# Kernel tuning notes

Measured on AMD Instinct MI355X. Metric: run time of the kernel, lower is better.

Reference implementation:

```python
import jax, jax.numpy as jnp
import numpy as np

B, C, T, V, P = 32, 64, 512, 54, 4
EPS = 1e-5


def setup_inputs() -> dict:
    key = jax.random.key(0)
    ks = jax.random.split(key, 5)
    x = jax.random.normal(ks[0], (B, C, T, V), dtype=jnp.float32)
    A = jax.random.uniform(ks[1], (P, V, V), dtype=jnp.float32)
    gweights = jax.random.normal(ks[2], (P, V, V), dtype=jnp.float32)
    W = jax.random.normal(ks[3], (P, C, C), dtype=jnp.float32) * 0.05  # (P, C_out, C_in)
    b = jax.random.normal(ks[4], (P, C), dtype=jnp.float32) * 0.05
    gamma = jnp.ones((C,), dtype=jnp.float32)
    beta = jnp.zeros((C,), dtype=jnp.float32)
    return {"x": x, "A": A, "gweights": gweights, "W": W, "b": b,
            "gamma": gamma, "beta": beta}


def reference(x, A, gweights, W, b, gamma, beta):
    # x: (B, C_in, T, V)
    Aeff = A * gweights  # (P, V, V), learned-weighted adjacency
    # per-part graph aggregation (x @ A_p) followed by 1x1 conv, summed over parts
    # out[b,o,t,v] = sum_p sum_c sum_u x[b,c,t,u] * Aeff[p,u,v] * W[p,o,c] + sum_p b[p,o]
    y = jnp.einsum('bctu,puv,poc->botv', x, Aeff, W, optimize=True)
    y = y + jnp.sum(b, axis=0)[None, :, None, None]
    # BatchNorm2d in training mode: batch stats over (B, T, V) per channel
    mean = jnp.mean(y, axis=(0, 2, 3), keepdims=True)
    var = jnp.mean(jnp.square(y - mean), axis=(0, 2, 3), keepdims=True)
    y = (y - mean) * jax.lax.rsqrt(var + EPS)
    y = y * gamma[None, :, None, None] + beta[None, :, None, None]
    y = jax.nn.relu(y)
    # temporal_conv is Identity (kernel_size=None); residual shortcut is Identity (C_in==C_out)
    return y + x
```

## Files before the change

### kernel.cpp

```cpp
#include <hip/hip_runtime.h>
#include <hip/hip_bf16.h>


typedef __bf16 bf16_t;
typedef __bf16 bf16x8 __attribute__((ext_vector_type(8)));
typedef __bf16 bf16x4 __attribute__((ext_vector_type(4)));
typedef float  f32x4  __attribute__((ext_vector_type(4)));
typedef unsigned int uint32;

static __device__ __forceinline__ f32x4 mfma16(bf16x8 a, bf16x8 b, f32x4 c) {
  return __builtin_amdgcn_mfma_f32_16x16x32_bf16(a, b, c, 0, 0, 0);
}
static __device__ __forceinline__ uint32 pk2(float a, float b) {
  union { __bf16 h; unsigned short u; } ua, ub;
  ua.h = (__bf16)a; ub.h = (__bf16)b;
  return (uint32)ua.u | ((uint32)ub.u << 16);
}
static __device__ __forceinline__ float bflo(uint32 u) {
  union { uint32 u; float f; } r; r.u = u << 16; return r.f;
}
static __device__ __forceinline__ float bfhi(uint32 u) {
  union { uint32 u; float f; } r; r.u = u & 0xffff0000u; return r.f;
}

__global__ __launch_bounds__(256) void k_prep(
    const float* __restrict__ A, const float* __restrict__ g,
    const float* __restrict__ W, const float* __restrict__ bias,
    bf16_t* __restrict__ W2, bf16_t* __restrict__ Ae,
    float* __restrict__ bsum, float* __restrict__ stats) {
  int i = blockIdx.x * 256 + threadIdx.x;
  if (i < 16384) {
    int o = i >> 8, k = i & 255, p = k >> 6, c = k & 63;
    W2[i] = (bf16_t)W[p * 4096 + o * 64 + c];
  }
  if (i < 224 * 64) {
    int pv = i >> 6, u = i & 63;
    int p = pv / 56, v = pv - p * 56;
    float val = 0.f;
    if (v < 54 && u < 54) {
      int idx = (p * 54 + u) * 54 + v;
      val = A[idx] * g[idx];
    }
    Ae[i] = (bf16_t)val;
  }
  if (i < 64) {
    float s = 0.f;
    for (int p = 0; p < 4; ++p) s += bias[p * 64 + i];
    bsum[i] = s;
  }
  if (i < 8192) stats[i] = 0.f;
}

__global__ __launch_bounds__(256) void k_cast(const float* __restrict__ x,
                                              bf16_t* __restrict__ xbf) {
  const size_t i = (size_t)blockIdx.x * 256 + threadIdx.x;
  const float4 a = ((const float4*)x)[2 * i];
  const float4 b = ((const float4*)x)[2 * i + 1];
  union { uint32 u[4]; uint4 v; } r;
  r.u[0] = pk2(a.x, a.y); r.u[1] = pk2(a.z, a.w);
  r.u[2] = pk2(b.x, b.y); r.u[3] = pk2(b.z, b.w);
  ((uint4*)xbf)[i] = r.v;
}

#define ZS  264
#define XSS 72

__global__ __launch_bounds__(256, 3) void k_pass1_bf(
    const bf16_t* __restrict__ xbf, const bf16_t* __restrict__ W2,
    const bf16_t* __restrict__ Ae, const float* __restrict__ bsum,
    bf16_t* __restrict__ yprev, float* __restrict__ stats) {
  __shared__ bf16_t Zt[64 * ZS];
  __shared__ bf16_t Xs[64 * XSS];
  __shared__ __align__(16) bf16_t Ys[64 * 54];

  const int tid  = threadIdx.x;
  const int bid  = blockIdx.x;
  const int b    = bid >> 7;
  const int t0   = (bid & 127) << 2;
  const int w    = tid >> 6;
  const int L    = tid & 63;
  const int quad = L >> 4;
  const int l15  = L & 15;

  for (int i = tid; i < 8 * ZS / 2; i += 256)
    ((uint32*)(Zt + 56 * ZS))[i] = 0u;

  bf16x8 wf[8];
  #pragma unroll
  for (int kk = 0; kk < 8; ++kk)
    wf[kk] = *(const bf16x8*)(W2 + (((w << 4) + l15) << 8) + (kk << 5) + (quad << 3));

  int zoff[14];
  #pragma unroll
  for (int n = 0; n < 14; ++n) {
    int pv = (n << 4) + l15;
    int p = pv / 56;
    int v = pv - p * 56;
    zoff[n] = v * ZS + (p << 6) + (w << 4) + (quad << 2);
  }

  const int oc  = (w << 4) + l15;
  const float bsv = bsum[oc];
  float ssum = 0.f, ssq = 0.f;

  const int  f2   = tid & 31;
  const bool ldon = f2 < 27;
  const bf16_t* xgb = xbf + ((size_t)(b << 6) + (tid >> 5)) * 27648 + (f2 << 1);
  uint32* xsd = (uint32*)((char*)Xs + (tid >> 5) * (XSS * 2) + (f2 << 2));

  uint32 pfu[8];
  #pragma unroll
  for (int j = 0; j < 8; ++j) pfu[j] = 0u;
  if (ldon) {
    #pragma unroll
    for (int j = 0; j < 8; ++j)
      pfu[j] = *(const uint32*)(xgb + (size_t)j * 221184 + (size_t)t0 * 54);
  }

  for (int tt = 0; tt < 4; ++tt) {
    const int t = t0 + tt;

    #pragma unroll
    for (int j = 0; j < 8; ++j) xsd[j * 288] = pfu[j];

    __syncthreads();

    const bf16_t* xr = Xs + oc * XSS;
    bf16x8 xa0 = *(const bf16x8*)(xr + (quad << 3));
    bf16x8 xa1 = *(const bf16x8*)(xr + 32 + (quad << 3));
    #pragma unroll
    for (int n = 0; n < 14; ++n) {
      const bf16_t* ar = Ae + (((n << 4) + l15) << 6) + (quad << 3);
      f32x4 acc = {0.f, 0.f, 0.f, 0.f};
      acc = mfma16(xa0, *(const bf16x8*)(ar), acc);
      acc = mfma16(xa1, *(const bf16x8*)(ar + 32), acc);
      uint32* dst = (uint32*)(Zt + zoff[n]);
      dst[0] = pk2(acc[0], acc[1]);
      dst[1] = pk2(acc[2], acc[3]);
    }

    __syncthreads();

    if (ldon && tt < 3) {
      #pragma unroll
      for (int j = 0; j < 8; ++j)
        pfu[j] = *(const uint32*)(xgb + (size_t)j * 221184 + (size_t)(t + 1) * 54);
    }

    #pragma unroll
    for (int mi = 0; mi < 4; ++mi) {
      f32x4 acc = {0.f, 0.f, 0.f, 0.f};
      #pragma unroll
      for (int kk = 0; kk < 8; ++kk) {
        bf16x8 za = *(const bf16x8*)(Zt + ((mi << 4) + l15) * ZS
                                        + (kk << 5) + (quad << 3));
        acc = mfma16(za, wf[kk], acc);
      }
      const int v0 = (mi << 4) + (quad << 2);
      if (v0 + 3 < 54) {
        float y0 = acc[0] + bsv, y1 = acc[1] + bsv, y2 = acc[2] + bsv, y3 = acc[3] + bsv;
        uint32* d = (uint32*)(Ys + oc * 54 + v0);
        d[0] = pk2(y0, y1); d[1] = pk2(y2, y3);
        ssum += y0 + y1 + y2 + y3;
        ssq  += y0 * y0 + y1 * y1 + y2 * y2 + y3 * y3;
      } else if (v0 == 52) {
        float y0 = acc[0] + bsv, y1 = acc[1] + bsv;
        *(uint32*)(Ys + oc * 54 + v0) = pk2(y0, y1);
        ssum += y0 + y1;
        ssq  += y0 * y0 + y1 * y1;
      }
    }

    __syncthreads();
    const uint4* ys4 = (const uint4*)Ys;
    uint4* yp4 = (uint4*)((uint32*)yprev + (size_t)bid * 6912 + (size_t)tt * 1728);
    yp4[tid] = ys4[tid];
    if (tid < 176) yp4[256 + tid] = ys4[256 + tid];
  }

  ssum += __shfl_xor(ssum, 16); ssq += __shfl_xor(ssq, 16);
  ssum += __shfl_xor(ssum, 32); ssq += __shfl_xor(ssq, 32);
  if (L < 16) {
    float* sb = stats + (bid & 63) * 128;
    atomicAdd(&sb[oc], ssum);
    atomicAdd(&sb[64 + oc], ssq);
  }
}

__global__ __launch_bounds__(256, 3) void k_pass1_fp32(
    const float* __restrict__ x, const bf16_t* __restrict__ W2,
    const bf16_t* __restrict__ Ae, const float* __restrict__ bsum,
    float* __restrict__ yprev, float* __restrict__ stats) {
  __shared__ bf16_t Zt[64 * ZS];
  __shared__ bf16_t Xs[64 * XSS];

  const int tid  = threadIdx.x;
  const int bid  = blockIdx.x;
  const int b    = bid >> 7;
  const int t0   = (bid & 127) << 2;
  const int w    = tid >> 6;
  const int L    = tid & 63;
  const int quad = L >> 4;
  const int l15  = L & 15;

  for (int i = tid; i < 8 * ZS / 2; i += 256)
    ((uint32*)(Zt + 56 * ZS))[i] = 0u;

  bf16x8 wf[8];
  #pragma unroll
  for (int kk = 0; kk < 8; ++kk)
    wf[kk] = *(const bf16x8*)(W2 + (((w << 4) + l15) << 8) + (kk << 5) + (quad << 3));

  int zoff[14];
  #pragma unroll
  for (int n = 0; n < 14; ++n) {
    int pv = (n << 4) + l15;
    int p = pv / 56;
    int v = pv - p * 56;
    zoff[n] = v * ZS + (p << 6) + (w << 4) + (quad << 2);
  }

  const int oc  = (w << 4) + l15;
  const float bsv = bsum[oc];
  float ssum = 0.f, ssq = 0.f;

  const int  f2   = tid & 31;
  const bool ldon = f2 < 27;
  const size_t gbase = ((size_t)(b << 6) + (tid >> 5)) * 27648 + ((size_t)f2 << 1);
  uint32* xsd = (uint32*)((char*)Xs + (tid >> 5) * (XSS * 2) + (f2 << 2));

  float2 pf[8];
  #pragma unroll
  for (int j = 0; j < 8; ++j) pf[j] = make_float2(0.f, 0.f);
  if (ldon) {
    #pragma unroll
    for (int j = 0; j < 8; ++j)
      pf[j] = *(const float2*)(x + gbase + (size_t)j * 221184 + (size_t)t0 * 54);
  }

  for (int tt = 0; tt < 4; ++tt) {
    const int t = t0 + tt;
    #pragma unroll
    for (int j = 0; j < 8; ++j) xsd[j * 288] = pk2(pf[j].x, pf[j].y);
    __syncthreads();

    const bf16_t* xr = Xs + oc * XSS;
    bf16x8 xa0 = *(const bf16x8*)(xr + (quad << 3));
    bf16x8 xa1 = *(const bf16x8*)(xr + 32 + (quad << 3));
    #pragma unroll
    for (int n = 0; n < 14; ++n) {
      const bf16_t* ar = Ae + (((n << 4) + l15) << 6) + (quad << 3);
      f32x4 acc = {0.f, 0.f, 0.f, 0.f};
      acc = mfma16(xa0, *(const bf16x8*)(ar), acc);
      acc = mfma16(xa1, *(const bf16x8*)(ar + 32), acc);
      uint32* dst = (uint32*)(Zt + zoff[n]);
      dst[0] = pk2(acc[0], acc[1]);
      dst[1] = pk2(acc[2], acc[3]);
    }
    __syncthreads();

    if (ldon && tt < 3) {
      #pragma unroll
      for (int j = 0; j < 8; ++j)
        pf[j] = *(const float2*)(x + gbase + (size_t)j * 221184 + (size_t)(t + 1) * 54);
    }

    const size_t obase = (((size_t)((b << 6) + oc) << 9) + (size_t)t) * 54;
    #pragma unroll
    for (int mi = 0; mi < 4; ++mi) {
      f32x4 acc = {0.f, 0.f, 0.f, 0.f};
      #pragma unroll
      for (int kk = 0; kk < 8; ++kk) {
        bf16x8 za = *(const bf16x8*)(Zt + ((mi << 4) + l15) * ZS
                                        + (kk << 5) + (quad << 3));
        acc = mfma16(za, wf[kk], acc);
      }
      const int v0 = (mi << 4) + (quad << 2);
      if (v0 + 3 < 54) {
        float y0 = acc[0] + bsv, y1 = acc[1] + bsv, y2 = acc[2] + bsv, y3 = acc[3] + bsv;
        float2* d = (float2*)(yprev + obase + v0);
        d[0] = make_float2(y0, y1); d[1] = make_float2(y2, y3);
        ssum += y0 + y1 + y2 + y3;
        ssq  += y0 * y0 + y1 * y1 + y2 * y2 + y3 * y3;
      } else if (v0 == 52) {
        float y0 = acc[0] + bsv, y1 = acc[1] + bsv;
        *(float2*)(yprev + obase + v0) = make_float2(y0, y1);
        ssum += y0 + y1;
        ssq  += y0 * y0 + y1 * y1;
      }
    }
    __syncthreads();
  }

  ssum += __shfl_xor(ssum, 16); ssq += __shfl_xor(ssq, 16);
  ssum += __shfl_xor(ssum, 32); ssq += __shfl_xor(ssq, 32);
  if (L < 16) {
    float* sb = stats + (bid & 63) * 128;
    atomicAdd(&sb[oc], ssum);
    atomicAdd(&sb[64 + oc], ssq);
  }
}

__global__ void k_finalize(const float* __restrict__ gamma, const float* __restrict__ beta,
                           const float* __restrict__ stats, float* __restrict__ ac) {
  int o = threadIdx.x;
  if (o >= 64) return;
  float S = 0.f, Q = 0.f;
  for (int buf = 0; buf < 64; ++buf) {
    S += stats[buf * 128 + o];
    Q += stats[buf * 128 + 64 + o];
  }
  const float inv = 1.0f / 884736.0f;
  float mean = S * inv;
  float var  = Q * inv - mean * mean;
  float a = gamma[o] * rsqrtf(var + 1e-5f);
  ac[o] = a;
  ac[64 + o] = beta[o] - mean * a;
}

__global__ __launch_bounds__(256) void k_pass2_lin(
    const float* __restrict__ x, const float* __restrict__ ac,
    const void* __restrict__ yprev, float* __restrict__ out) {
  __shared__ float acS[128];
  const int tid = threadIdx.x;
  const int bid = blockIdx.x;
  if (tid < 128) acS[tid] = ac[tid];
  __syncthreads();

  const int b  = bid >> 7;
  const int t0 = (bid & 127) << 2;
  const uint32* yp = (const uint32*)yprev + (size_t)bid * 6912;
  const float* xb  = x + (size_t)b * 1769472;
  float* ob        = out + (size_t)b * 1769472;

  #pragma unroll 3
  for (int k = 0; k < 27; ++k) {
    const int d  = (k << 8) + tid;
    const int e0 = d << 1;
    const unsigned tt = (unsigned)e0 / 3456u;
    const unsigned r  = (unsigned)e0 - tt * 3456u;
    const unsigned ocv = r / 54u;
    const unsigned v   = r - ocv * 54u;
    const uint32 u = yp[d];
    const float a = acS[ocv], cc = acS[64 + ocv];
    const size_t xi = (size_t)ocv * 27648 + (size_t)(t0 + tt) * 54 + v;
    const float2 xv = *(const float2*)(xb + xi);
    float2 o2;
    o2.x = fmaxf(fmaf(a, bflo(u), cc), 0.f) + xv.x;
    o2.y = fmaxf(fmaf(a, bfhi(u), cc), 0.f) + xv.y;
    *(float2*)(ob + xi) = o2;
  }
}

__global__ __launch_bounds__(256) void k_pass2_fb(const float* __restrict__ x,
                                                  const float* __restrict__ ac,
                                                  const float* __restrict__ yprev,
                                                  float* __restrict__ out) {
  const int slab = blockIdx.y;
  const int o = slab & 63;
  const size_t base = (size_t)slab * 27648 + (size_t)(((blockIdx.x << 8) + threadIdx.x) << 2);
  const float a = ac[o], c = ac[64 + o];
  float4 yp = *(const float4*)(yprev + base);
  float4 xv = *(const float4*)(x + base);
  float4 r;
  r.x = fmaxf(fmaf(a, yp.x, c), 0.f) + xv.x;
  r.y = fmaxf(fmaf(a, yp.y, c), 0.f) + xv.y;
  r.z = fmaxf(fmaf(a, yp.z, c), 0.f) + xv.z;
  r.w = fmaxf(fmaf(a, yp.w, c), 0.f) + xv.w;
  *(float4*)(out + base) = r;
}

extern "C" void kernel_launch(void* const* d_in, const int* in_sizes, int n_in,
                              void* d_out, int out_size, void* d_ws, size_t ws_size,
                              hipStream_t stream) {
  const float* x     = (const float*)d_in[0];
  const float* A     = (const float*)d_in[1];
  const float* g     = (const float*)d_in[2];
  const float* W     = (const float*)d_in[3];
  const float* bias  = (const float*)d_in[4];
  const float* gamma = (const float*)d_in[5];
  const float* beta  = (const float*)d_in[6];

  char* ws = (char*)d_ws;
  bf16_t* W2    = (bf16_t*)(ws + 0);
  bf16_t* Ae    = (bf16_t*)(ws + 32768);
  float*  bsum  = (float*)(ws + 61440);
  float*  stats = (float*)(ws + 61696);
  float*  ac    = (float*)(ws + 94464);
  const size_t XBF_OFF   = 98304;
  const size_t XBF_BYTES = (size_t)32 * 64 * 512 * 54 * 2;
  const size_t YP_OFF    = XBF_OFF + XBF_BYTES;
  float* out = (float*)d_out;

  k_prep<<<64, 256, 0, stream>>>(A, g, W, bias, W2, Ae, bsum, stats);

  if (ws_size >= YP_OFF + XBF_BYTES + 4096) {
    bf16_t* xbf  = (bf16_t*)(ws + XBF_OFF);
    bf16_t* ypre = (bf16_t*)(ws + YP_OFF);
    k_cast<<<27648, 256, 0, stream>>>(x, xbf);
    k_pass1_bf<<<4096, 256, 0, stream>>>(xbf, W2, Ae, bsum, ypre, stats);
    k_finalize<<<1, 64, 0, stream>>>(gamma, beta, stats, ac);
    k_pass2_lin<<<4096, 256, 0, stream>>>(x, ac, ypre, out);
  } else {
    k_pass1_fp32<<<4096, 256, 0, stream>>>(x, W2, Ae, bsum, out, stats);
    k_finalize<<<1, 64, 0, stream>>>(gamma, beta, stats, ac);
    k_pass2_fb<<<dim3(27, 2048), 256, 0, stream>>>(x, ac, out, out);
  }
}
```

Baseline: 717.8 us.

## Cast x into per-block contiguous tiles and shrink pass1 to two timesteps

The cast kernel now writes x in bf16 into contiguous per-block tiles of 64 channels by 2 timesteps, so pass1 can load its whole input slab with coalesced 16-byte loads instead of strided per-channel gathers and register prefetch. Pass1 now handles 2 timesteps per block across 8192 blocks and writes y directly to global memory, dropping the LDS staging buffer and its copy-out. This cuts shared memory and sync overhead but gives up the prefetch overlap. The cast now does strided float2 reads, and the direct y stores are narrower and less coalesced.

Result: slower. 792.5 us (+10.4%).

```diff
diff --git a/kernel.cpp b/kernel.cpp
--- a/kernel.cpp
+++ b/kernel.cpp
@@ -51,38 +51,58 @@
   if (i < 8192) stats[i] = 0.f;
 }
 
-__global__ __launch_bounds__(256) void k_cast(const float* __restrict__ x,
-                                              bf16_t* __restrict__ xbf) {
-  const size_t i = (size_t)blockIdx.x * 256 + threadIdx.x;
-  const float4 a = ((const float4*)x)[2 * i];
-  const float4 b = ((const float4*)x)[2 * i + 1];
-  union { uint32 u[4]; uint4 v; } r;
-  r.u[0] = pk2(a.x, a.y); r.u[1] = pk2(a.z, a.w);
-  r.u[2] = pk2(b.x, b.y); r.u[3] = pk2(b.z, b.w);
-  ((uint4*)xbf)[i] = r.v;
-}
-
-#define ZS  264
-#define XSS 72
-
-__global__ __launch_bounds__(256, 3) void k_pass1_bf(
-    const bf16_t* __restrict__ xbf, const bf16_t* __restrict__ W2,
+__global__ __launch_bounds__(256) void k_cast_blk(const float* __restrict__ x,
+                                                  bf16_t* __restrict__ xblk) {
+  const int tid = threadIdx.x;
+  const int bid = blockIdx.x;
+  const int b   = bid >> 8;
+  const int t0  = (bid & 255) << 1;
+  const float* xb = x + (size_t)b * 1769472;
+  uint32* dstD = (uint32*)xblk + (size_t)bid * 3456;
+  #pragma unroll
+  for (int r = 0; r < 7; ++r) {
+    int d = (r << 8) + tid;
+    if (d < 1728) {
+      int c  = d / 27;
+      int u2 = d - c * 27;
+      const float* s = xb + (size_t)c * 27648 + (size_t)t0 * 54 + (u2 << 1);
+      float2 a0 = *(const float2*)s;
+      float2 a1 = *(const float2*)(s + 54);
+      dstD[d]        = pk2(a0.x, a0.y);
+      dstD[d + 1728] = pk2(a1.x, a1.y);
+    }
+  }
+}
+
+#define ZS 264
+
+__global__ __launch_bounds__(256, 3) void k_pass1_blk(
+    const bf16_t* __restrict__ xblk, const bf16_t* __restrict__ W2,
     const bf16_t* __restrict__ Ae, const float* __restrict__ bsum,
     bf16_t* __restrict__ yprev, float* __restrict__ stats) {
+  __shared__ __align__(16) bf16_t Xs[2 * 64 * 54 + 64];
   __shared__ bf16_t Zt[64 * ZS];
-  __shared__ bf16_t Xs[64 * XSS];
-  __shared__ __align__(16) bf16_t Ys[64 * 54];
 
   const int tid  = threadIdx.x;
   const int bid  = blockIdx.x;
-  const int b    = bid >> 7;
-  const int t0   = (bid & 127) << 2;
+  const int b    = bid >> 8;
+  const int t0   = (bid & 255) << 1;
   const int w    = tid >> 6;
   const int L    = tid & 63;
   const int quad = L >> 4;
   const int l15  = L & 15;
 
-  for (int i = tid; i < 8 * ZS / 2; i += 256)
+  {
+    const uint4* src = (const uint4*)(xblk + (size_t)bid * 6912);
+    uint4* xs4 = (uint4*)Xs;
+    #pragma unroll
+    for (int r = 0; r < 4; ++r) {
+      int i4 = (r << 8) + tid;
+      if (i4 < 864) xs4[i4] = src[i4];
+    }
+  }
+
+  for (int i = tid; i < 1056; i += 256)
     ((uint32*)(Zt + 56 * ZS))[i] = 0u;
 
   bf16x8 wf[8];
@@ -103,31 +123,21 @@
   const float bsv = bsum[oc];
   float ssum = 0.f, ssq = 0.f;
 
-  const int  f2   = tid & 31;
-  const bool ldon = f2 < 27;
-  const bf16_t* xgb = xbf + ((size_t)(b << 6) + (tid >> 5)) * 27648 + (f2 << 1);
-  uint32* xsd = (uint32*)((char*)Xs + (tid >> 5) * (XSS * 2) + (f2 << 2));
-
-  uint32 pfu[8];
-  #pragma unroll
-  for (int j = 0; j < 8; ++j) pfu[j] = 0u;
-  if (ldon) {
-    #pragma unroll
-    for (int j = 0; j < 8; ++j)
-      pfu[j] = *(const uint32*)(xgb + (size_t)j * 221184 + (size_t)t0 * 54);
-  }
-
-  for (int tt = 0; tt < 4; ++tt) {
+  __syncthreads();
+
+  const uint32* XsD = (const uint32*)Xs;
+
+  for (int tt = 0; tt < 2; ++tt) {
     const int t = t0 + tt;
 
-    #pragma unroll
-    for (int j = 0; j < 8; ++j) xsd[j * 288] = pfu[j];
-
-    __syncthreads();
-
-    const bf16_t* xr = Xs + oc * XSS;
-    bf16x8 xa0 = *(const bf16x8*)(xr + (quad << 3));
-    bf16x8 xa1 = *(const bf16x8*)(xr + 32 + (quad << 3));
+    const int xbase = ((tt << 6) + oc) * 27 + (quad << 2);
+    union { uint32 u[4]; bf16x8 v; } ua0, ua1;
+    ua0.u[0] = XsD[xbase];      ua0.u[1] = XsD[xbase + 1];
+    ua0.u[2] = XsD[xbase + 2];  ua0.u[3] = XsD[xbase + 3];
+    ua1.u[0] = XsD[xbase + 16]; ua1.u[1] = XsD[xbase + 17];
+    ua1.u[2] = XsD[xbase + 18]; ua1.u[3] = XsD[xbase + 19];
+    const bf16x8 xa0 = ua0.v, xa1 = ua1.v;
+
     #pragma unroll
     for (int n = 0; n < 14; ++n) {
       const bf16_t* ar = Ae + (((n << 4) + l15) << 6) + (quad << 3);
@@ -141,12 +151,8 @@
 
     __syncthreads();
 
-    if (ldon && tt < 3) {
-      #pragma unroll
-      for (int j = 0; j < 8; ++j)
-        pfu[j] = *(const uint32*)(xgb + (size_t)j * 221184 + (size_t)(t + 1) * 54);
-    }
-
+    const size_t ybase = (size_t)((b << 7) + (t >> 2)) * 13824
+                       + (size_t)(t & 3) * 3456 + (size_t)oc * 54;
     #pragma unroll
     for (int mi = 0; mi < 4; ++mi) {
       f32x4 acc = {0.f, 0.f, 0.f, 0.f};
@@ -159,23 +165,19 @@
       const int v0 = (mi << 4) + (quad << 2);
       if (v0 + 3 < 54) {
         float y0 = acc[0] + bsv, y1 = acc[1] + bsv, y2 = acc[2] + bsv, y3 = acc[3] + bsv;
-        uint32* d = (uint32*)(Ys + oc * 54 + v0);
+        uint32* d = (uint32*)(yprev + ybase + v0);
         d[0] = pk2(y0, y1); d[1] = pk2(y2, y3);
         ssum += y0 + y1 + y2 + y3;
         ssq  += y0 * y0 + y1 * y1 + y2 * y2 + y3 * y3;
       } else if (v0 == 52) {
         float y0 = acc[0] + bsv, y1 = acc[1] + bsv;
-        *(uint32*)(Ys + oc * 54 + v0) = pk2(y0, y1);
+        *(uint32*)(yprev + ybase + v0) = pk2(y0, y1);
         ssum += y0 + y1;
         ssq  += y0 * y0 + y1 * y1;
       }
     }
 
     __syncthreads();
-    const uint4* ys4 = (const uint4*)Ys;
-    uint4* yp4 = (uint4*)((uint32*)yprev + (size_t)bid * 6912 + (size_t)tt * 1728);
-    yp4[tid] = ys4[tid];
-    if (tid < 176) yp4[256 + tid] = ys4[256 + tid];
   }
 
   ssum += __shfl_xor(ssum, 16); ssq += __shfl_xor(ssq, 16);
@@ -187,6 +189,7 @@
   }
 }
 
+#define XSS 72
 __global__ __launch_bounds__(256, 3) void k_pass1_fp32(
     const float* __restrict__ x, const bf16_t* __restrict__ W2,
     const bf16_t* __restrict__ Ae, const float* __restrict__ bsum,
@@ -203,7 +206,7 @@
   const int quad = L >> 4;
   const int l15  = L & 15;
 
-  for (int i = tid; i < 8 * ZS / 2; i += 256)
+  for (int i = tid; i < 1056; i += 256)
     ((uint32*)(Zt + 56 * ZS))[i] = 0u;
 
   bf16x8 wf[8];
@@ -395,10 +398,10 @@
   k_prep<<<64, 256, 0, stream>>>(A, g, W, bias, W2, Ae, bsum, stats);
 
   if (ws_size >= YP_OFF + XBF_BYTES + 4096) {
-    bf16_t* xbf  = (bf16_t*)(ws + XBF_OFF);
+    bf16_t* xblk = (bf16_t*)(ws + XBF_OFF);
     bf16_t* ypre = (bf16_t*)(ws + YP_OFF);
-    k_cast<<<27648, 256, 0, stream>>>(x, xbf);
-    k_pass1_bf<<<4096, 256, 0, stream>>>(xbf, W2, Ae, bsum, ypre, stats);
+    k_cast_blk<<<8192, 256, 0, stream>>>(x, xblk);
+    k_pass1_blk<<<8192, 256, 0, stream>>>(xblk, W2, Ae, bsum, ypre, stats);
     k_finalize<<<1, 64, 0, stream>>>(gamma, beta, stats, ac);
     k_pass2_lin<<<4096, 256, 0, stream>>>(x, ac, ypre, out);
   } else {
```
